# Optimization experiments

Measured on AMD Instinct MI355X. Metric: run time of the kernel, lower is better.

The kernel has to match this reference:

```python
import jax, jax.numpy as jnp
import numpy as np

N, M, C = 32768, 8192, 128
K = 3            # number of interpolation neighbors (PointNet++/RepSurf FP)
EPS_BN = 1e-5    # torch BatchNorm1d default eps
EPS_D = 1e-8     # RepSurf dist_recip eps


def setup_inputs() -> dict:
    key = jax.random.key(0)
    ks = jax.random.split(key, 16)
    s = 0.05
    inp = {
        "pos1": jax.random.normal(ks[0], (N, 3), jnp.float32),
        "pos2": jax.random.normal(ks[1], (M, 3), jnp.float32),
        "feat2": jax.random.normal(ks[2], (M, C), jnp.float32),
    }
    # MLP stack [128,128,128]: Linear + BatchNorm1d (gamma/beta) per layer
    for i in range(3):
        inp[f"W{i}"] = jax.random.normal(ks[3 + i], (C, C), jnp.float32) * s
        inp[f"b{i}"] = jnp.zeros((C,), jnp.float32)
        inp[f"g{i}"] = jnp.ones((C,), jnp.float32)
        inp[f"be{i}"] = jnp.zeros((C,), jnp.float32)
    return inp


def _lin_bn_relu(x, W, b, g, be):
    # Linear -> BatchNorm1d (training-mode batch stats, biased var) -> ReLU
    y = x @ W.T + b
    m = y.mean(axis=0)
    v = y.var(axis=0)
    return jax.nn.relu((y - m) * jax.lax.rsqrt(v + EPS_BN) * g + be)


def reference(pos1, pos2, feat2, W0, b0, g0, be0, W1, b1, g1, be1, W2, b2, g2, be2):
    # squared pairwise distances [N, M] (memory-bound: 1 GB fp32)
    d = ((pos1 ** 2).sum(-1, keepdims=True)
         + (pos2 ** 2).sum(-1)[None, :]
         - 2.0 * (pos1 @ pos2.T))
    neg_d, idx = jax.lax.top_k(-d, K)          # 3 nearest neighbors
    dk = jnp.maximum(-neg_d, 0.0)              # [N, K] squared dists
    w = 1.0 / (dk + EPS_D)
    w = w / w.sum(-1, keepdims=True)           # inverse-distance weights
    # gather neighbor features and interpolate: [N, K, C] -> [N, C]
    interp = jnp.einsum('nkc,nk->nc', feat2[idx], w)
    x = _lin_bn_relu(interp, W0, b0, g0, be0)
    x = _lin_bn_relu(x, W1, b1, g1, be1)
    x = _lin_bn_relu(x, W2, b2, g2, be2)
    return x
```

## Files before the change

### kernel.cpp

```cpp
#include <hip/hip_runtime.h>
#include <math.h>

#define NQ 32768
#define MC 8192
#define CC 128
#define EPS_BN 1e-5f
#define EPS_D  1e-8

#define DBL_BIG 1e300
#define IDX_BIG 0x7fffffff

#define QB  64
#define TB  512
#define NW  8
#define CH  2048
#define HM  (MC / 2)
#define NCH (HM / CH)
#define SLC (CH / NW)
#define KMASK 0xFFFFE000u
#define IMASK 0x1FFFu
#define NSURV 64
#define KNN_B ((NQ / QB) * 2)
#define GEMM_B (NQ / 64)
#define NGRP 8

typedef __attribute__((ext_vector_type(8))) short bf16x8;
typedef __attribute__((ext_vector_type(4))) float floatx4;
typedef unsigned short ushort_t;

__device__ __forceinline__ unsigned umin_(unsigned a, unsigned b) { return a < b ? a : b; }
__device__ __forceinline__ unsigned umax_(unsigned a, unsigned b) { return a > b ? a : b; }
#define KSWAP(a, b) { unsigned t_ = umin_(a, b); b = umax_(a, b); a = t_; }

__device__ __forceinline__ unsigned bf16pair(float a, float b) {
    unsigned ua = __float_as_uint(a); ua = (ua + 0x7FFFu + ((ua >> 16) & 1u)) >> 16;
    unsigned ub = __float_as_uint(b); ub = (ub + 0x7FFFu + ((ub >> 16) & 1u)) >> 16;
    return ua | (ub << 16);
}
__device__ __forceinline__ ushort_t bf16one(float a) {
    unsigned ua = __float_as_uint(a);
    return (ushort_t)((ua + 0x7FFFu + ((ua >> 16) & 1u)) >> 16);
}
__device__ __forceinline__ float bflo(unsigned u) { return __uint_as_float(u << 16); }
__device__ __forceinline__ float bfhi(unsigned u) { return __uint_as_float(u & 0xFFFF0000u); }

__global__ __launch_bounds__(TB) void knn_kernel(const float* __restrict__ pos1,
                                                 const float* __restrict__ pos2,
                                                 unsigned* __restrict__ skeys,
                                                 const float* __restrict__ W0,
                                                 const float* __restrict__ W1,
                                                 const float* __restrict__ W2,
                                                 ushort_t* __restrict__ Wbf,
                                                 float* __restrict__ stats) {
    __shared__ __align__(16) float4 sp4[CH * 3 / 4];
    __shared__ unsigned skey[QB][NW * 4];

    if (blockIdx.x >= KNN_B) {
        const int pb = blockIdx.x - KNN_B;
        const int f = pb * TB + threadIdx.x;
        const float* Ws[3] = {W0, W1, W2};
#pragma unroll
        for (int l = 0; l < 3; ++l) {
            const float4 v = ((const float4*)Ws[l])[f];
            unsigned* dst = (unsigned*)(Wbf + (size_t)l * CC * CC);
            dst[f * 2 + 0] = bf16pair(v.x, v.y);
            dst[f * 2 + 1] = bf16pair(v.z, v.w);
        }
        if (pb == 0)
            for (int i = threadIdx.x; i < 3 * NGRP * 256; i += TB) stats[i] = 0.f;
        return;
    }

    const int half = blockIdx.x & 1;
    const int bq   = blockIdx.x >> 1;
    const int wv = threadIdx.x >> 6;
    const int ln = threadIdx.x & 63;
    const int q  = bq * QB + ln;

    const float px = pos1[q * 3 + 0];
    const float py = pos1[q * 3 + 1];
    const float pz = pos1[q * 3 + 2];

    unsigned k0 = 0xFFFFFFFFu, k1 = 0xFFFFFFFFu, k2 = 0xFFFFFFFFu, k3 = 0xFFFFFFFFu;

    for (int c0 = 0; c0 < NCH; ++c0) {
        const int cb = half * HM + c0 * CH;
        __syncthreads();
        {
            const float4* g4 = (const float4*)(pos2 + (size_t)cb * 3);
#pragma unroll
            for (int i = threadIdx.x; i < CH * 3 / 4; i += TB) sp4[i] = g4[i];
        }
        __syncthreads();
        const float4* b4 = sp4 + wv * (SLC * 3 / 4);
        const int jb = cb + wv * SLC;
#pragma unroll 4
        for (int gi = 0; gi < SLC / 4; ++gi) {
            const float4 A = b4[gi * 3 + 0];
            const float4 B = b4[gi * 3 + 1];
            const float4 Cv = b4[gi * 3 + 2];
            const int j = jb + gi * 4;
            const float cx[4] = {A.x, A.w, B.z, Cv.y};
            const float cy[4] = {A.y, B.x, B.w, Cv.z};
            const float cz[4] = {A.z, B.y, Cv.x, Cv.w};
            unsigned e0, e1, e2, e3;
            {
                float dx = px - cx[0], dy = py - cy[0], dz = pz - cz[0];
                e0 = (__float_as_uint(fmaf(dx, dx, fmaf(dy, dy, dz * dz))) & KMASK) | (unsigned)(j + 0);
                dx = px - cx[1]; dy = py - cy[1]; dz = pz - cz[1];
                e1 = (__float_as_uint(fmaf(dx, dx, fmaf(dy, dy, dz * dz))) & KMASK) | (unsigned)(j + 1);
                dx = px - cx[2]; dy = py - cy[2]; dz = pz - cz[2];
                e2 = (__float_as_uint(fmaf(dx, dx, fmaf(dy, dy, dz * dz))) & KMASK) | (unsigned)(j + 2);
                dx = px - cx[3]; dy = py - cy[3]; dz = pz - cz[3];
                e3 = (__float_as_uint(fmaf(dx, dx, fmaf(dy, dy, dz * dz))) & KMASK) | (unsigned)(j + 3);
            }
            KSWAP(e0, e1); KSWAP(e2, e3); KSWAP(e0, e2); KSWAP(e1, e3); KSWAP(e1, e2);
            unsigned m0 = umin_(k0, e3), m1 = umin_(k1, e2);
            unsigned m2 = umin_(k2, e1), m3 = umin_(k3, e0);
            KSWAP(m0, m2); KSWAP(m1, m3); KSWAP(m0, m1); KSWAP(m2, m3);
            k0 = m0; k1 = m1; k2 = m2; k3 = m3;
        }
    }
    skey[ln][wv * 4 + 0] = k0;
    skey[ln][wv * 4 + 1] = k1;
    skey[ln][wv * 4 + 2] = k2;
    skey[ln][wv * 4 + 3] = k3;
    __syncthreads();

#pragma unroll
    for (int t = threadIdx.x * 4; t < threadIdx.x * 4 + 4; ++t) {
        const int ql = t >> 5, slot = t & 31;
        skeys[(size_t)(bq * QB + ql) * NSURV + half * 32 + slot] = skey[ql][slot];
    }
}

template <int MODE>
__global__ __launch_bounds__(256) void gemm_mfma(const void* __restrict__ Xsrc_,
                                                 const unsigned* __restrict__ skeys,
                                                 const float* __restrict__ pos1,
                                                 const float* __restrict__ pos2,
                                                 const float* __restrict__ statsIn,
                                                 const float* __restrict__ gIn,
                                                 const float* __restrict__ beIn,
                                                 const ushort_t* __restrict__ Wb,
                                                 const float* __restrict__ bias,
                                                 ushort_t* __restrict__ Y,
                                                 float* __restrict__ statsOut) {
    __shared__ __align__(16) short xa[64][136];
    __shared__ __align__(16) short wb[128][136];
    __shared__ float blk_s[CC], blk_q[CC];
    __shared__ float sc_l[CC], sh_l[CC];

    const int row0 = blockIdx.x * 64;

    if constexpr (MODE == 0) {
        const float* feat2 = (const float*)Xsrc_;
        __shared__ int   lidx[QB][3];
        __shared__ float lw[QB][3];
        {
            double* rrd = (double*)&xa[0][0];
            int*    rri = (int*)&wb[0][0];
            const int ql = threadIdx.x >> 2;
            const int pp = threadIdx.x & 3;
            const int qg = row0 + ql;
            const double qx = (double)pos1[qg * 3 + 0];
            const double qy = (double)pos1[qg * 3 + 1];
            const double qz = (double)pos1[qg * 3 + 2];
            double b0 = DBL_BIG, b1 = DBL_BIG, b2 = DBL_BIG;
            int    j0 = IDX_BIG, j1 = IDX_BIG, j2 = IDX_BIG;
            const uint4* kp = (const uint4*)(skeys + (size_t)qg * NSURV + pp * 16);
#pragma unroll
            for (int gi = 0; gi < 4; ++gi) {
                const uint4 kk = kp[gi];
                const unsigned ks[4] = {kk.x, kk.y, kk.z, kk.w};
#pragma unroll
                for (int u = 0; u < 4; ++u) {
                    const int id = (int)(ks[u] & IMASK);
                    const double x = (double)pos2[id * 3 + 0];
                    const double y = (double)pos2[id * 3 + 1];
                    const double z = (double)pos2[id * 3 + 2];
                    const double ax = qx - x, ay = qy - y, az = qz - z;
                    const double d = ax * ax + ay * ay + az * az;
                    const bool l2 = (d < b2) || (d == b2 && id < j2);
                    if (l2) {
                        const bool l1 = (d < b1) || (d == b1 && id < j1);
                        const bool l0 = (d < b0) || (d == b0 && id < j0);
                        b2 = l1 ? b1 : d;              j2 = l1 ? j1 : id;
                        b1 = l1 ? (l0 ? b0 : d) : b1;  j1 = l1 ? (l0 ? j0 : id) : j1;
                        b0 = l0 ? d : b0;              j0 = l0 ? id : j0;
                    }
                }
            }
            const int base = (ql * 4 + pp) * 3;
            rrd[base + 0] = b0; rri[base + 0] = j0;
            rrd[base + 1] = b1; rri[base + 1] = j1;
            rrd[base + 2] = b2; rri[base + 2] = j2;
            __syncthreads();
            if (threadIdx.x < QB) {
                const int qq = threadIdx.x;
                double c0 = DBL_BIG, c1 = DBL_BIG, c2 = DBL_BIG;
                int    i0 = IDX_BIG, i1 = IDX_BIG, i2 = IDX_BIG;
#pragma unroll
                for (int s = 0; s < 12; ++s) {
                    const double d = rrd[qq * 12 + s];
                    const int   id = rri[qq * 12 + s];
                    const bool l2 = (d < c2) || (d == c2 && id < i2);
                    if (l2) {
                        const bool l1 = (d < c1) || (d == c1 && id < i1);
                        const bool l0 = (d < c0) || (d == c0 && id < i0);
                        c2 = l1 ? c1 : d;              i2 = l1 ? i1 : id;
                        c1 = l1 ? (l0 ? c0 : d) : c1;  i1 = l1 ? (l0 ? i0 : id) : i1;
                        c0 = l0 ? d : c0;              i0 = l0 ? id : i0;
                    }
                }
                const double r0 = 1.0 / (c0 + EPS_D);
                const double r1 = 1.0 / (c1 + EPS_D);
                const double r2 = 1.0 / (c2 + EPS_D);
                const double inv = 1.0 / (r0 + r1 + r2);
                lidx[qq][0] = i0; lidx[qq][1] = i1; lidx[qq][2] = i2;
                lw[qq][0] = (float)(r0 * inv);
                lw[qq][1] = (float)(r1 * inv);
                lw[qq][2] = (float)(r2 * inv);
            }
            __syncthreads();
        }
        if (threadIdx.x < CC) { blk_s[threadIdx.x] = 0.f; blk_q[threadIdx.x] = 0.f; }
#pragma unroll
        for (int e = threadIdx.x; e < 64 * 32; e += 256) {
            const int r = e >> 5, c4 = e & 31;
            const int i0 = lidx[r][0], i1 = lidx[r][1], i2 = lidx[r][2];
            const float w0 = lw[r][0], w1 = lw[r][1], w2 = lw[r][2];
            const float4 f0 = *(const float4*)&feat2[(size_t)i0 * CC + c4 * 4];
            const float4 f1 = *(const float4*)&feat2[(size_t)i1 * CC + c4 * 4];
            const float4 f2 = *(const float4*)&feat2[(size_t)i2 * CC + c4 * 4];
            float4 v;
            v.x = w0 * f0.x + w1 * f1.x + w2 * f2.x;
            v.y = w0 * f0.y + w1 * f1.y + w2 * f2.y;
            v.z = w0 * f0.z + w1 * f1.z + w2 * f2.z;
            v.w = w0 * f0.w + w1 * f1.w + w2 * f2.w;
            unsigned* dst = (unsigned*)&xa[r][0];
            dst[c4 * 2 + 0] = bf16pair(v.x, v.y);
            dst[c4 * 2 + 1] = bf16pair(v.z, v.w);
        }
    } else {
        const ushort_t* Xbf = (const ushort_t*)Xsrc_;
        if (threadIdx.x < CC) {
            const int c = threadIdx.x;
            float s = 0.f, q = 0.f;
#pragma unroll
            for (int gr = 0; gr < NGRP; ++gr) {
                s += statsIn[gr * 256 + c];
                q += statsIn[gr * 256 + CC + c];
            }
            const float m = s * (1.f / (float)NQ);
            const float v = fmaf(-m, m, q * (1.f / (float)NQ));
            const float rstd = rsqrtf(v + EPS_BN);
            const float scl = gIn[c] * rstd;
            sc_l[c] = scl;
            sh_l[c] = fmaf(-m, scl, beIn[c]);
            blk_s[c] = 0.f; blk_q[c] = 0.f;
        }
        __syncthreads();
#pragma unroll
        for (int e = threadIdx.x; e < 64 * 16; e += 256) {
            const int r = e >> 4, c8 = e & 15;
            const uint4 u = *(const uint4*)&Xbf[(size_t)(row0 + r) * CC + c8 * 8];
            const float4 s0 = *(const float4*)&sc_l[c8 * 8];
            const float4 s1 = *(const float4*)&sc_l[c8 * 8 + 4];
            const float4 h0 = *(const float4*)&sh_l[c8 * 8];
            const float4 h1 = *(const float4*)&sh_l[c8 * 8 + 4];
            const float v0 = fmaxf(fmaf(bflo(u.x), s0.x, h0.x), 0.f);
            const float v1 = fmaxf(fmaf(bfhi(u.x), s0.y, h0.y), 0.f);
            const float v2 = fmaxf(fmaf(bflo(u.y), s0.z, h0.z), 0.f);
            const float v3 = fmaxf(fmaf(bfhi(u.y), s0.w, h0.w), 0.f);
            const float v4 = fmaxf(fmaf(bflo(u.z), s1.x, h1.x), 0.f);
            const float v5 = fmaxf(fmaf(bfhi(u.z), s1.y, h1.y), 0.f);
            const float v6 = fmaxf(fmaf(bflo(u.w), s1.z, h1.z), 0.f);
            const float v7 = fmaxf(fmaf(bfhi(u.w), s1.w, h1.w), 0.f);
            uint4 o;
            o.x = bf16pair(v0, v1); o.y = bf16pair(v2, v3);
            o.z = bf16pair(v4, v5); o.w = bf16pair(v6, v7);
            *(uint4*)&xa[r][c8 * 8] = o;
        }
    }
#pragma unroll
    for (int e = threadIdx.x; e < 128 * 16; e += 256) {
        const int co = e >> 4, seg = e & 15;
        *(float4*)&wb[co][seg * 8] = *(const float4*)&Wb[(size_t)co * CC + seg * 8];
    }
    __syncthreads();

    const int lane = threadIdx.x & 63;
    const int wv = threadIdx.x >> 6;
    const int nn = lane & 15;
    const int quad = lane >> 4;

    floatx4 acc[8] = {};

    const short* arow = &xa[wv * 16 + nn][0];
#pragma unroll
    for (int ks = 0; ks < 4; ++ks) {
        const bf16x8 a = *(const bf16x8*)(arow + ks * 32 + quad * 8);
#pragma unroll
        for (int ct = 0; ct < 8; ++ct) {
            const bf16x8 b = *(const bf16x8*)(&wb[ct * 16 + nn][0] + ks * 32 + quad * 8);
            acc[ct] = __builtin_amdgcn_mfma_f32_16x16x32_bf16(a, b, acc[ct], 0, 0, 0);
        }
    }

#pragma unroll
    for (int ct = 0; ct < 8; ++ct) {
        const float bv = bias[ct * 16 + nn];
        float s = 0.f, qv = 0.f;
#pragma unroll
        for (int r = 0; r < 4; ++r) {
            acc[ct][r] += bv;
            s += acc[ct][r];
            qv = fmaf(acc[ct][r], acc[ct][r], qv);
        }
#pragma unroll
        for (int r = 0; r < 4; ++r)
            Y[(size_t)(row0 + wv * 16 + quad * 4 + r) * CC + ct * 16 + nn] = bf16one(acc[ct][r]);
        s += __shfl_xor(s, 16, 64); s += __shfl_xor(s, 32, 64);
        qv += __shfl_xor(qv, 16, 64); qv += __shfl_xor(qv, 32, 64);
        if (quad == 0) {
            atomicAdd(&blk_s[ct * 16 + nn], s);
            atomicAdd(&blk_q[ct * 16 + nn], qv);
        }
    }
    __syncthreads();
    {
        const int ch = threadIdx.x;
        const float v = (ch < CC) ? blk_s[ch] : blk_q[ch - CC];
        atomicAdd(&statsOut[(blockIdx.x & (NGRP - 1)) * 256 + ch], v);
    }
}

__global__ __launch_bounds__(256) void bn_final(const ushort_t* __restrict__ Y,
                                                const float* __restrict__ statsIn,
                                                const float* __restrict__ g,
                                                const float* __restrict__ be,
                                                float* __restrict__ out) {
    __shared__ float sc_l[CC], sh_l[CC];
    if (threadIdx.x < CC) {
        const int c = threadIdx.x;
        float s = 0.f, q = 0.f;
#pragma unroll
        for (int gr = 0; gr < NGRP; ++gr) {
            s += statsIn[gr * 256 + c];
            q += statsIn[gr * 256 + CC + c];
        }
        const float m = s * (1.f / (float)NQ);
        const float v = fmaf(-m, m, q * (1.f / (float)NQ));
        const float rstd = rsqrtf(v + EPS_BN);
        const float scl = g[c] * rstd;
        sc_l[c] = scl;
        sh_l[c] = fmaf(-m, scl, be[c]);
    }
    __syncthreads();
    const int base = blockIdx.x * 1024 + threadIdx.x;
#pragma unroll
    for (int it = 0; it < 4; ++it) {
        const int i8 = base + it * 256;
        const int c8 = (i8 & 15) * 8;
        const uint4 u = *(const uint4*)&Y[(size_t)i8 * 8];
        const float4 s0 = *(const float4*)&sc_l[c8];
        const float4 s1 = *(const float4*)&sc_l[c8 + 4];
        const float4 h0 = *(const float4*)&sh_l[c8];
        const float4 h1 = *(const float4*)&sh_l[c8 + 4];
        float4 o0, o1;
        o0.x = fmaxf(fmaf(bflo(u.x), s0.x, h0.x), 0.f);
        o0.y = fmaxf(fmaf(bfhi(u.x), s0.y, h0.y), 0.f);
        o0.z = fmaxf(fmaf(bflo(u.y), s0.z, h0.z), 0.f);
        o0.w = fmaxf(fmaf(bfhi(u.y), s0.w, h0.w), 0.f);
        o1.x = fmaxf(fmaf(bflo(u.z), s1.x, h1.x), 0.f);
        o1.y = fmaxf(fmaf(bfhi(u.z), s1.y, h1.y), 0.f);
        o1.z = fmaxf(fmaf(bflo(u.w), s1.z, h1.z), 0.f);
        o1.w = fmaxf(fmaf(bfhi(u.w), s1.w, h1.w), 0.f);
        ((float4*)out)[i8 * 2 + 0] = o0;
        ((float4*)out)[i8 * 2 + 1] = o1;
    }
}

extern "C" void kernel_launch(void* const* d_in, const int* in_sizes, int n_in,
                              void* d_out, int out_size, void* d_ws, size_t ws_size,
                              hipStream_t stream) {
    (void)in_sizes; (void)n_in; (void)out_size; (void)ws_size;

    const float* pos1  = (const float*)d_in[0];
    const float* pos2  = (const float*)d_in[1];
    const float* feat2 = (const float*)d_in[2];
    const float* Wl[3]  = {(const float*)d_in[3], (const float*)d_in[7],  (const float*)d_in[11]};
    const float* bl[3]  = {(const float*)d_in[4], (const float*)d_in[8],  (const float*)d_in[12]};
    const float* gl[3]  = {(const float*)d_in[5], (const float*)d_in[9],  (const float*)d_in[13]};
    const float* bel[3] = {(const float*)d_in[6], (const float*)d_in[10], (const float*)d_in[14]};

    float* ws = (float*)d_ws;
    ushort_t* B0 = (ushort_t*)ws;
    ushort_t* B1 = B0 + (size_t)NQ * CC;
    unsigned* skeys = (unsigned*)(B1 + (size_t)NQ * CC);
    float* stats = (float*)(skeys + (size_t)NQ * NSURV);
    ushort_t* Wbf = (ushort_t*)(stats + 3 * NGRP * 256);

    float* st0 = stats + 0 * NGRP * 256;
    float* st1 = stats + 1 * NGRP * 256;
    float* st2 = stats + 2 * NGRP * 256;

    knn_kernel<<<KNN_B + 8, TB, 0, stream>>>(pos1, pos2, skeys,
                                             Wl[0], Wl[1], Wl[2], Wbf, stats);
    gemm_mfma<0><<<GEMM_B, 256, 0, stream>>>(feat2, skeys, pos1, pos2,
                                             nullptr, nullptr, nullptr,
                                             Wbf + 0 * CC * CC, bl[0], B0, st0);
    gemm_mfma<1><<<GEMM_B, 256, 0, stream>>>(B0, nullptr, nullptr, nullptr,
                                             st0, gl[0], bel[0],
                                             Wbf + 1 * CC * CC, bl[1], B1, st1);
    gemm_mfma<1><<<GEMM_B, 256, 0, stream>>>(B1, nullptr, nullptr, nullptr,
                                             st1, gl[1], bel[1],
                                             Wbf + 2 * CC * CC, bl[2], B0, st2);
    bn_final<<<GEMM_B, 256, 0, stream>>>(B0, st2, gl[2], bel[2], (float*)d_out);
}
```

Before: 204.6 us.

## Fuse three MLP layers and final BN into one persistent kernel with grid barriers

Replaces the three gemm launches and the final BN kernel with a single persistent kernel of 512 blocks. Each block keeps its 64-row activation tile in registers and LDS across layers and uses a software grid barrier on atomic counters to wait for the global BatchNorm statistics. This removes the bf16 intermediate round trips through global memory and three kernel launches. It depends on all 512 blocks being co-resident (launch_bounds 256,2), and the spin barrier adds synchronisation latency; the barrier counter is zeroed each call by the first kernel.

```diff
diff --git a/kernel.cpp b/kernel.cpp
--- a/kernel.cpp
+++ b/kernel.cpp
@@ -41,8 +41,6 @@
     unsigned ua = __float_as_uint(a);
     return (ushort_t)((ua + 0x7FFFu + ((ua >> 16) & 1u)) >> 16);
 }
-__device__ __forceinline__ float bflo(unsigned u) { return __uint_as_float(u << 16); }
-__device__ __forceinline__ float bfhi(unsigned u) { return __uint_as_float(u & 0xFFFF0000u); }
 
 __global__ __launch_bounds__(TB) void knn_kernel(const float* __restrict__ pos1,
                                                  const float* __restrict__ pos2,
@@ -67,7 +65,7 @@
             dst[f * 2 + 1] = bf16pair(v.z, v.w);
         }
         if (pb == 0)
-            for (int i = threadIdx.x; i < 3 * NGRP * 256; i += TB) stats[i] = 0.f;
+            for (int i = threadIdx.x; i < 3 * NGRP * 256 + 8; i += TB) stats[i] = 0.f;
         return;
     }
 
@@ -134,251 +132,270 @@
     }
 }
 
-template <int MODE>
-__global__ __launch_bounds__(256) void gemm_mfma(const void* __restrict__ Xsrc_,
-                                                 const unsigned* __restrict__ skeys,
-                                                 const float* __restrict__ pos1,
-                                                 const float* __restrict__ pos2,
-                                                 const float* __restrict__ statsIn,
-                                                 const float* __restrict__ gIn,
-                                                 const float* __restrict__ beIn,
-                                                 const ushort_t* __restrict__ Wb,
-                                                 const float* __restrict__ bias,
-                                                 ushort_t* __restrict__ Y,
-                                                 float* __restrict__ statsOut) {
+struct MlpP {
+    const float* feat2;
+    const unsigned* skeys;
+    const float* pos1;
+    const float* pos2;
+    const ushort_t* Wbf;
+    const float* bias0; const float* bias1; const float* bias2;
+    const float* g0;    const float* g1;    const float* g2;
+    const float* be0;   const float* be1;   const float* be2;
+    float* stats;
+    unsigned* bar;
+    float* out;
+};
+
+__device__ __forceinline__ void gbar(unsigned* cnt, unsigned* gen) {
+    __syncthreads();
+    if (threadIdx.x == 0) {
+        const unsigned g = __hip_atomic_load(gen, __ATOMIC_RELAXED, __HIP_MEMORY_SCOPE_AGENT);
+        const unsigned old = __hip_atomic_fetch_add(cnt, 1u, __ATOMIC_ACQ_REL, __HIP_MEMORY_SCOPE_AGENT);
+        if (old == (unsigned)(GEMM_B - 1)) {
+            __hip_atomic_store(cnt, 0u, __ATOMIC_RELAXED, __HIP_MEMORY_SCOPE_AGENT);
+            __hip_atomic_store(gen, g + 1u, __ATOMIC_RELEASE, __HIP_MEMORY_SCOPE_AGENT);
+        } else {
+            while (__hip_atomic_load(gen, __ATOMIC_ACQUIRE, __HIP_MEMORY_SCOPE_AGENT) == g)
+                __builtin_amdgcn_s_sleep(8);
+        }
+    }
+    __syncthreads();
+}
+
+__global__ __launch_bounds__(256, 2) void mlp_persist(MlpP P) {
     __shared__ __align__(16) short xa[64][136];
     __shared__ __align__(16) short wb[128][136];
     __shared__ float blk_s[CC], blk_q[CC];
     __shared__ float sc_l[CC], sh_l[CC];
+    __shared__ int   lidx[QB][3];
+    __shared__ float lw[QB][3];
 
     const int row0 = blockIdx.x * 64;
-
-    if constexpr (MODE == 0) {
-        const float* feat2 = (const float*)Xsrc_;
-        __shared__ int   lidx[QB][3];
-        __shared__ float lw[QB][3];
-        {
-            double* rrd = (double*)&xa[0][0];
-            int*    rri = (int*)&wb[0][0];
-            const int ql = threadIdx.x >> 2;
-            const int pp = threadIdx.x & 3;
-            const int qg = row0 + ql;
-            const double qx = (double)pos1[qg * 3 + 0];
-            const double qy = (double)pos1[qg * 3 + 1];
-            const double qz = (double)pos1[qg * 3 + 2];
-            double b0 = DBL_BIG, b1 = DBL_BIG, b2 = DBL_BIG;
-            int    j0 = IDX_BIG, j1 = IDX_BIG, j2 = IDX_BIG;
-            const uint4* kp = (const uint4*)(skeys + (size_t)qg * NSURV + pp * 16);
-#pragma unroll
-            for (int gi = 0; gi < 4; ++gi) {
-                const uint4 kk = kp[gi];
-                const unsigned ks[4] = {kk.x, kk.y, kk.z, kk.w};
-#pragma unroll
-                for (int u = 0; u < 4; ++u) {
-                    const int id = (int)(ks[u] & IMASK);
-                    const double x = (double)pos2[id * 3 + 0];
-                    const double y = (double)pos2[id * 3 + 1];
-                    const double z = (double)pos2[id * 3 + 2];
-                    const double ax = qx - x, ay = qy - y, az = qz - z;
-                    const double d = ax * ax + ay * ay + az * az;
-                    const bool l2 = (d < b2) || (d == b2 && id < j2);
-                    if (l2) {
-                        const bool l1 = (d < b1) || (d == b1 && id < j1);
-                        const bool l0 = (d < b0) || (d == b0 && id < j0);
-                        b2 = l1 ? b1 : d;              j2 = l1 ? j1 : id;
-                        b1 = l1 ? (l0 ? b0 : d) : b1;  j1 = l1 ? (l0 ? j0 : id) : j1;
-                        b0 = l0 ? d : b0;              j0 = l0 ? id : j0;
-                    }
-                }
-            }
-            const int base = (ql * 4 + pp) * 3;
-            rrd[base + 0] = b0; rri[base + 0] = j0;
-            rrd[base + 1] = b1; rri[base + 1] = j1;
-            rrd[base + 2] = b2; rri[base + 2] = j2;
-            __syncthreads();
-            if (threadIdx.x < QB) {
-                const int qq = threadIdx.x;
-                double c0 = DBL_BIG, c1 = DBL_BIG, c2 = DBL_BIG;
-                int    i0 = IDX_BIG, i1 = IDX_BIG, i2 = IDX_BIG;
-#pragma unroll
-                for (int s = 0; s < 12; ++s) {
-                    const double d = rrd[qq * 12 + s];
-                    const int   id = rri[qq * 12 + s];
-                    const bool l2 = (d < c2) || (d == c2 && id < i2);
-                    if (l2) {
-                        const bool l1 = (d < c1) || (d == c1 && id < i1);
-                        const bool l0 = (d < c0) || (d == c0 && id < i0);
-                        c2 = l1 ? c1 : d;              i2 = l1 ? i1 : id;
-                        c1 = l1 ? (l0 ? c0 : d) : c1;  i1 = l1 ? (l0 ? i0 : id) : i1;
-                        c0 = l0 ? d : c0;              i0 = l0 ? id : i0;
-                    }
-                }
-                const double r0 = 1.0 / (c0 + EPS_D);
-                const double r1 = 1.0 / (c1 + EPS_D);
-                const double r2 = 1.0 / (c2 + EPS_D);
-                const double inv = 1.0 / (r0 + r1 + r2);
-                lidx[qq][0] = i0; lidx[qq][1] = i1; lidx[qq][2] = i2;
-                lw[qq][0] = (float)(r0 * inv);
-                lw[qq][1] = (float)(r1 * inv);
-                lw[qq][2] = (float)(r2 * inv);
-            }
-            __syncthreads();
-        }
-        if (threadIdx.x < CC) { blk_s[threadIdx.x] = 0.f; blk_q[threadIdx.x] = 0.f; }
-#pragma unroll
-        for (int e = threadIdx.x; e < 64 * 32; e += 256) {
-            const int r = e >> 5, c4 = e & 31;
-            const int i0 = lidx[r][0], i1 = lidx[r][1], i2 = lidx[r][2];
-            const float w0 = lw[r][0], w1 = lw[r][1], w2 = lw[r][2];
-            const float4 f0 = *(const float4*)&feat2[(size_t)i0 * CC + c4 * 4];
-            const float4 f1 = *(const float4*)&feat2[(size_t)i1 * CC + c4 * 4];
-            const float4 f2 = *(const float4*)&feat2[(size_t)i2 * CC + c4 * 4];
-            float4 v;
-            v.x = w0 * f0.x + w1 * f1.x + w2 * f2.x;
-            v.y = w0 * f0.y + w1 * f1.y + w2 * f2.y;
-            v.z = w0 * f0.z + w1 * f1.z + w2 * f2.z;
-            v.w = w0 * f0.w + w1 * f1.w + w2 * f2.w;
-            unsigned* dst = (unsigned*)&xa[r][0];
-            dst[c4 * 2 + 0] = bf16pair(v.x, v.y);
-            dst[c4 * 2 + 1] = bf16pair(v.z, v.w);
-        }
-    } else {
-        const ushort_t* Xbf = (const ushort_t*)Xsrc_;
-        if (threadIdx.x < CC) {
-            const int c = threadIdx.x;
-            float s = 0.f, q = 0.f;
-#pragma unroll
-            for (int gr = 0; gr < NGRP; ++gr) {
-                s += statsIn[gr * 256 + c];
-                q += statsIn[gr * 256 + CC + c];
-            }
-            const float m = s * (1.f / (float)NQ);
-            const float v = fmaf(-m, m, q * (1.f / (float)NQ));
-            const float rstd = rsqrtf(v + EPS_BN);
-            const float scl = gIn[c] * rstd;
-            sc_l[c] = scl;
-            sh_l[c] = fmaf(-m, scl, beIn[c]);
-            blk_s[c] = 0.f; blk_q[c] = 0.f;
-        }
-        __syncthreads();
-#pragma unroll
-        for (int e = threadIdx.x; e < 64 * 16; e += 256) {
-            const int r = e >> 4, c8 = e & 15;
-            const uint4 u = *(const uint4*)&Xbf[(size_t)(row0 + r) * CC + c8 * 8];
-            const float4 s0 = *(const float4*)&sc_l[c8 * 8];
-            const float4 s1 = *(const float4*)&sc_l[c8 * 8 + 4];
-            const float4 h0 = *(const float4*)&sh_l[c8 * 8];
-            const float4 h1 = *(const float4*)&sh_l[c8 * 8 + 4];
-            const float v0 = fmaxf(fmaf(bflo(u.x), s0.x, h0.x), 0.f);
-            const float v1 = fmaxf(fmaf(bfhi(u.x), s0.y, h0.y), 0.f);
-            const float v2 = fmaxf(fmaf(bflo(u.y), s0.z, h0.z), 0.f);
-            const float v3 = fmaxf(fmaf(bfhi(u.y), s0.w, h0.w), 0.f);
-            const float v4 = fmaxf(fmaf(bflo(u.z), s1.x, h1.x), 0.f);
-            const float v5 = fmaxf(fmaf(bfhi(u.z), s1.y, h1.y), 0.f);
-            const float v6 = fmaxf(fmaf(bflo(u.w), s1.z, h1.z), 0.f);
-            const float v7 = fmaxf(fmaf(bfhi(u.w), s1.w, h1.w), 0.f);
-            uint4 o;
-            o.x = bf16pair(v0, v1); o.y = bf16pair(v2, v3);
-            o.z = bf16pair(v4, v5); o.w = bf16pair(v6, v7);
-            *(uint4*)&xa[r][c8 * 8] = o;
-        }
-    }
-#pragma unroll
-    for (int e = threadIdx.x; e < 128 * 16; e += 256) {
-        const int co = e >> 4, seg = e & 15;
-        *(float4*)&wb[co][seg * 8] = *(const float4*)&Wb[(size_t)co * CC + seg * 8];
-    }
-    __syncthreads();
-
     const int lane = threadIdx.x & 63;
     const int wv = threadIdx.x >> 6;
     const int nn = lane & 15;
     const int quad = lane >> 4;
 
-    floatx4 acc[8] = {};
-
-    const short* arow = &xa[wv * 16 + nn][0];
-#pragma unroll
-    for (int ks = 0; ks < 4; ++ks) {
-        const bf16x8 a = *(const bf16x8*)(arow + ks * 32 + quad * 8);
+    {
+        double* rrd = (double*)&xa[0][0];
+        int*    rri = (int*)&wb[0][0];
+        const int ql = threadIdx.x >> 2;
+        const int pp = threadIdx.x & 3;
+        const int qg = row0 + ql;
+        const double qx = (double)P.pos1[qg * 3 + 0];
+        const double qy = (double)P.pos1[qg * 3 + 1];
+        const double qz = (double)P.pos1[qg * 3 + 2];
+        double b0 = DBL_BIG, b1 = DBL_BIG, b2 = DBL_BIG;
+        int    j0 = IDX_BIG, j1 = IDX_BIG, j2 = IDX_BIG;
+        const uint4* kp = (const uint4*)(P.skeys + (size_t)qg * NSURV + pp * 16);
+#pragma unroll
+        for (int gi = 0; gi < 4; ++gi) {
+            const uint4 kk = kp[gi];
+            const unsigned ks[4] = {kk.x, kk.y, kk.z, kk.w};
+#pragma unroll
+            for (int u = 0; u < 4; ++u) {
+                const int id = (int)(ks[u] & IMASK);
+                const double x = (double)P.pos2[id * 3 + 0];
+                const double y = (double)P.pos2[id * 3 + 1];
+                const double z = (double)P.pos2[id * 3 + 2];
+                const double ax = qx - x, ay = qy - y, az = qz - z;
+                const double d = ax * ax + ay * ay + az * az;
+                const bool l2 = (d < b2) || (d == b2 && id < j2);
+                if (l2) {
+                    const bool l1 = (d < b1) || (d == b1 && id < j1);
+                    const bool l0 = (d < b0) || (d == b0 && id < j0);
+                    b2 = l1 ? b1 : d;              j2 = l1 ? j1 : id;
+                    b1 = l1 ? (l0 ? b0 : d) : b1;  j1 = l1 ? (l0 ? j0 : id) : j1;
+                    b0 = l0 ? d : b0;              j0 = l0 ? id : j0;
+                }
+            }
+        }
+        const int base = (ql * 4 + pp) * 3;
+        rrd[base + 0] = b0; rri[base + 0] = j0;
+        rrd[base + 1] = b1; rri[base + 1] = j1;
+        rrd[base + 2] = b2; rri[base + 2] = j2;
+        __syncthreads();
+        if (threadIdx.x < QB) {
+            const int qq = threadIdx.x;
+            double c0 = DBL_BIG, c1 = DBL_BIG, c2 = DBL_BIG;
+            int    i0 = IDX_BIG, i1 = IDX_BIG, i2 = IDX_BIG;
+#pragma unroll
+            for (int s = 0; s < 12; ++s) {
+                const double d = rrd[qq * 12 + s];
+                const int   id = rri[qq * 12 + s];
+                const bool l2 = (d < c2) || (d == c2 && id < i2);
+                if (l2) {
+                    const bool l1 = (d < c1) || (d == c1 && id < i1);
+                    const bool l0 = (d < c0) || (d == c0 && id < i0);
+                    c2 = l1 ? c1 : d;              i2 = l1 ? i1 : id;
+                    c1 = l1 ? (l0 ? c0 : d) : c1;  i1 = l1 ? (l0 ? i0 : id) : i1;
+                    c0 = l0 ? d : c0;              i0 = l0 ? id : i0;
+                }
+            }
+            const double r0 = 1.0 / (c0 + EPS_D);
+            const double r1 = 1.0 / (c1 + EPS_D);
+            const double r2 = 1.0 / (c2 + EPS_D);
+            const double inv = 1.0 / (r0 + r1 + r2);
+            lidx[qq][0] = i0; lidx[qq][1] = i1; lidx[qq][2] = i2;
+            lw[qq][0] = (float)(r0 * inv);
+            lw[qq][1] = (float)(r1 * inv);
+            lw[qq][2] = (float)(r2 * inv);
+        }
+        __syncthreads();
+    }
+
+#pragma unroll
+    for (int e = threadIdx.x; e < 64 * 32; e += 256) {
+        const int r = e >> 5, c4 = e & 31;
+        const int i0 = lidx[r][0], i1 = lidx[r][1], i2 = lidx[r][2];
+        const float w0 = lw[r][0], w1 = lw[r][1], w2 = lw[r][2];
+        const float4 f0 = *(const float4*)&P.feat2[(size_t)i0 * CC + c4 * 4];
+        const float4 f1 = *(const float4*)&P.feat2[(size_t)i1 * CC + c4 * 4];
+        const float4 f2 = *(const float4*)&P.feat2[(size_t)i2 * CC + c4 * 4];
+        float4 v;
+        v.x = w0 * f0.x + w1 * f1.x + w2 * f2.x;
+        v.y = w0 * f0.y + w1 * f1.y + w2 * f2.y;
+        v.z = w0 * f0.z + w1 * f1.z + w2 * f2.z;
+        v.w = w0 * f0.w + w1 * f1.w + w2 * f2.w;
+        unsigned* dst = (unsigned*)&xa[r][0];
+        dst[c4 * 2 + 0] = bf16pair(v.x, v.y);
+        dst[c4 * 2 + 1] = bf16pair(v.z, v.w);
+    }
+#pragma unroll
+    for (int e = threadIdx.x; e < 128 * 16; e += 256) {
+        const int co = e >> 4, seg = e & 15;
+        *(float4*)&wb[co][seg * 8] = *(const float4*)&P.Wbf[(size_t)co * CC + seg * 8];
+    }
+    __syncthreads();
+
+    const float* biasL[3] = {P.bias0, P.bias1, P.bias2};
+    const float* gL[3]    = {P.g0, P.g1, P.g2};
+    const float* beL[3]   = {P.be0, P.be1, P.be2};
+
+    floatx4 acc[8];
+#pragma unroll
+    for (int ct = 0; ct < 8; ++ct) acc[ct] = (floatx4){0.f, 0.f, 0.f, 0.f};
+    {
+        const short* arow = &xa[wv * 16 + nn][0];
+#pragma unroll
+        for (int ks = 0; ks < 4; ++ks) {
+            const bf16x8 a = *(const bf16x8*)(arow + ks * 32 + quad * 8);
+#pragma unroll
+            for (int ct = 0; ct < 8; ++ct) {
+                const bf16x8 b = *(const bf16x8*)(&wb[ct * 16 + nn][0] + ks * 32 + quad * 8);
+                acc[ct] = __builtin_amdgcn_mfma_f32_16x16x32_bf16(a, b, acc[ct], 0, 0, 0);
+            }
+        }
 #pragma unroll
         for (int ct = 0; ct < 8; ++ct) {
-            const bf16x8 b = *(const bf16x8*)(&wb[ct * 16 + nn][0] + ks * 32 + quad * 8);
-            acc[ct] = __builtin_amdgcn_mfma_f32_16x16x32_bf16(a, b, acc[ct], 0, 0, 0);
-        }
-    }
-
-#pragma unroll
-    for (int ct = 0; ct < 8; ++ct) {
-        const float bv = bias[ct * 16 + nn];
-        float s = 0.f, qv = 0.f;
-#pragma unroll
-        for (int r = 0; r < 4; ++r) {
-            acc[ct][r] += bv;
-            s += acc[ct][r];
-            qv = fmaf(acc[ct][r], acc[ct][r], qv);
-        }
-#pragma unroll
-        for (int r = 0; r < 4; ++r)
-            Y[(size_t)(row0 + wv * 16 + quad * 4 + r) * CC + ct * 16 + nn] = bf16one(acc[ct][r]);
-        s += __shfl_xor(s, 16, 64); s += __shfl_xor(s, 32, 64);
-        qv += __shfl_xor(qv, 16, 64); qv += __shfl_xor(qv, 32, 64);
-        if (quad == 0) {
-            atomicAdd(&blk_s[ct * 16 + nn], s);
-            atomicAdd(&blk_q[ct * 16 + nn], qv);
-        }
-    }
-    __syncthreads();
-    {
-        const int ch = threadIdx.x;
-        const float v = (ch < CC) ? blk_s[ch] : blk_q[ch - CC];
-        atomicAdd(&statsOut[(blockIdx.x & (NGRP - 1)) * 256 + ch], v);
-    }
-}
-
-__global__ __launch_bounds__(256) void bn_final(const ushort_t* __restrict__ Y,
-                                                const float* __restrict__ statsIn,
-                                                const float* __restrict__ g,
-                                                const float* __restrict__ be,
-                                                float* __restrict__ out) {
-    __shared__ float sc_l[CC], sh_l[CC];
-    if (threadIdx.x < CC) {
-        const int c = threadIdx.x;
-        float s = 0.f, q = 0.f;
-#pragma unroll
-        for (int gr = 0; gr < NGRP; ++gr) {
-            s += statsIn[gr * 256 + c];
-            q += statsIn[gr * 256 + CC + c];
-        }
-        const float m = s * (1.f / (float)NQ);
-        const float v = fmaf(-m, m, q * (1.f / (float)NQ));
-        const float rstd = rsqrtf(v + EPS_BN);
-        const float scl = g[c] * rstd;
-        sc_l[c] = scl;
-        sh_l[c] = fmaf(-m, scl, be[c]);
-    }
-    __syncthreads();
-    const int base = blockIdx.x * 1024 + threadIdx.x;
-#pragma unroll
-    for (int it = 0; it < 4; ++it) {
-        const int i8 = base + it * 256;
-        const int c8 = (i8 & 15) * 8;
-        const uint4 u = *(const uint4*)&Y[(size_t)i8 * 8];
-        const float4 s0 = *(const float4*)&sc_l[c8];
-        const float4 s1 = *(const float4*)&sc_l[c8 + 4];
-        const float4 h0 = *(const float4*)&sh_l[c8];
-        const float4 h1 = *(const float4*)&sh_l[c8 + 4];
-        float4 o0, o1;
-        o0.x = fmaxf(fmaf(bflo(u.x), s0.x, h0.x), 0.f);
-        o0.y = fmaxf(fmaf(bfhi(u.x), s0.y, h0.y), 0.f);
-        o0.z = fmaxf(fmaf(bflo(u.y), s0.z, h0.z), 0.f);
-        o0.w = fmaxf(fmaf(bfhi(u.y), s0.w, h0.w), 0.f);
-        o1.x = fmaxf(fmaf(bflo(u.z), s1.x, h1.x), 0.f);
-        o1.y = fmaxf(fmaf(bfhi(u.z), s1.y, h1.y), 0.f);
-        o1.z = fmaxf(fmaf(bflo(u.w), s1.z, h1.z), 0.f);
-        o1.w = fmaxf(fmaf(bfhi(u.w), s1.w, h1.w), 0.f);
-        ((float4*)out)[i8 * 2 + 0] = o0;
-        ((float4*)out)[i8 * 2 + 1] = o1;
+            const float bv = biasL[0][ct * 16 + nn];
+#pragma unroll
+            for (int r = 0; r < 4; ++r) acc[ct][r] += bv;
+        }
+    }
+
+    for (int l = 0; l < 3; ++l) {
+        float* stL = P.stats + l * NGRP * 256;
+        __syncthreads();
+        if (threadIdx.x < CC) { blk_s[threadIdx.x] = 0.f; blk_q[threadIdx.x] = 0.f; }
+        __syncthreads();
+#pragma unroll
+        for (int ct = 0; ct < 8; ++ct) {
+            float s = 0.f, qv = 0.f;
+#pragma unroll
+            for (int r = 0; r < 4; ++r) {
+                s += acc[ct][r];
+                qv = fmaf(acc[ct][r], acc[ct][r], qv);
+            }
+            s += __shfl_xor(s, 16, 64); s += __shfl_xor(s, 32, 64);
+            qv += __shfl_xor(qv, 16, 64); qv += __shfl_xor(qv, 32, 64);
+            if (quad == 0) {
+                atomicAdd(&blk_s[ct * 16 + nn], s);
+                atomicAdd(&blk_q[ct * 16 + nn], qv);
+            }
+        }
+        __syncthreads();
+        {
+            const int ch = threadIdx.x;
+            const float v = (ch < CC) ? blk_s[ch] : blk_q[ch - CC];
+            atomicAdd(&stL[(blockIdx.x & (NGRP - 1)) * 256 + ch], v);
+        }
+        gbar(P.bar, P.bar + 1);
+        if (threadIdx.x < CC) {
+            const int c = threadIdx.x;
+            float s = 0.f, q = 0.f;
+#pragma unroll
+            for (int gr = 0; gr < NGRP; ++gr) {
+                s += stL[gr * 256 + c];
+                q += stL[gr * 256 + CC + c];
+            }
+            const float m = s * (1.f / (float)NQ);
+            const float v = fmaf(-m, m, q * (1.f / (float)NQ));
+            const float rstd = rsqrtf(v + EPS_BN);
+            const float scl = gL[l][c] * rstd;
+            sc_l[c] = scl;
+            sh_l[c] = fmaf(-m, scl, beL[l][c]);
+        }
+        __syncthreads();
+
+        if (l < 2) {
+#pragma unroll
+            for (int ct = 0; ct < 8; ++ct) {
+                const int col = ct * 16 + nn;
+                const float scl = sc_l[col], shf = sh_l[col];
+#pragma unroll
+                for (int r = 0; r < 4; ++r) {
+                    const int row = wv * 16 + quad * 4 + r;
+                    const float v = fmaxf(fmaf(acc[ct][r], scl, shf), 0.f);
+                    ((ushort_t*)&xa[row][0])[col] = bf16one(v);
+                }
+            }
+            const ushort_t* Wp = P.Wbf + (size_t)(l + 1) * CC * CC;
+#pragma unroll
+            for (int e = threadIdx.x; e < 128 * 16; e += 256) {
+                const int co = e >> 4, seg = e & 15;
+                *(float4*)&wb[co][seg * 8] = *(const float4*)&Wp[(size_t)co * CC + seg * 8];
+            }
+            __syncthreads();
+#pragma unroll
+            for (int ct = 0; ct < 8; ++ct) acc[ct] = (floatx4){0.f, 0.f, 0.f, 0.f};
+            const short* arow = &xa[wv * 16 + nn][0];
+#pragma unroll
+            for (int ks = 0; ks < 4; ++ks) {
+                const bf16x8 a = *(const bf16x8*)(arow + ks * 32 + quad * 8);
+#pragma unroll
+                for (int ct = 0; ct < 8; ++ct) {
+                    const bf16x8 b = *(const bf16x8*)(&wb[ct * 16 + nn][0] + ks * 32 + quad * 8);
+                    acc[ct] = __builtin_amdgcn_mfma_f32_16x16x32_bf16(a, b, acc[ct], 0, 0, 0);
+                }
+            }
+#pragma unroll
+            for (int ct = 0; ct < 8; ++ct) {
+                const float bv = biasL[l + 1][ct * 16 + nn];
+#pragma unroll
+                for (int r = 0; r < 4; ++r) acc[ct][r] += bv;
+            }
+        } else {
+            float* wf = (float*)&wb[0][0];
+#pragma unroll
+            for (int ct = 0; ct < 8; ++ct) {
+                const int col = ct * 16 + nn;
+                const float scl = sc_l[col], shf = sh_l[col];
+#pragma unroll
+                for (int r = 0; r < 4; ++r) {
+                    const int row = wv * 16 + quad * 4 + r;
+                    wf[row * 132 + col] = fmaxf(fmaf(acc[ct][r], scl, shf), 0.f);
+                }
+            }
+            __syncthreads();
+#pragma unroll
+            for (int it = 0; it < 8; ++it) {
+                const int idx = it * 256 + threadIdx.x;
+                const int row = idx >> 5, c4 = idx & 31;
+                const float4 v = *(const float4*)&wf[row * 132 + c4 * 4];
+                *(float4*)&P.out[(size_t)(row0 + row) * CC + c4 * 4] = v;
+            }
+        }
     }
 }
 
@@ -396,26 +413,19 @@
     const float* bel[3] = {(const float*)d_in[6], (const float*)d_in[10], (const float*)d_in[14]};
 
     float* ws = (float*)d_ws;
-    ushort_t* B0 = (ushort_t*)ws;
-    ushort_t* B1 = B0 + (size_t)NQ * CC;
-    unsigned* skeys = (unsigned*)(B1 + (size_t)NQ * CC);
+    unsigned* skeys = (unsigned*)ws;
     float* stats = (float*)(skeys + (size_t)NQ * NSURV);
-    ushort_t* Wbf = (ushort_t*)(stats + 3 * NGRP * 256);
-
-    float* st0 = stats + 0 * NGRP * 256;
-    float* st1 = stats + 1 * NGRP * 256;
-    float* st2 = stats + 2 * NGRP * 256;
+    unsigned* bar = (unsigned*)(stats + 3 * NGRP * 256);
+    ushort_t* Wbf = (ushort_t*)(stats + 3 * NGRP * 256 + 8);
 
     knn_kernel<<<KNN_B + 8, TB, 0, stream>>>(pos1, pos2, skeys,
                                              Wl[0], Wl[1], Wl[2], Wbf, stats);
-    gemm_mfma<0><<<GEMM_B, 256, 0, stream>>>(feat2, skeys, pos1, pos2,
-                                             nullptr, nullptr, nullptr,
-                                             Wbf + 0 * CC * CC, bl[0], B0, st0);
-    gemm_mfma<1><<<GEMM_B, 256, 0, stream>>>(B0, nullptr, nullptr, nullptr,
-                                             st0, gl[0], bel[0],
-                                             Wbf + 1 * CC * CC, bl[1], B1, st1);
-    gemm_mfma<1><<<GEMM_B, 256, 0, stream>>>(B1, nullptr, nullptr, nullptr,
-                                             st1, gl[1], bel[1],
-                                             Wbf + 2 * CC * CC, bl[2], B0, st2);
-    bn_final<<<GEMM_B, 256, 0, stream>>>(B0, st2, gl[2], bel[2], (float*)d_out);
-}
+    MlpP P;
+    P.feat2 = feat2; P.skeys = skeys; P.pos1 = pos1; P.pos2 = pos2;
+    P.Wbf = Wbf;
+    P.bias0 = bl[0]; P.bias1 = bl[1]; P.bias2 = bl[2];
+    P.g0 = gl[0]; P.g1 = gl[1]; P.g2 = gl[2];
+    P.be0 = bel[0]; P.be1 = bel[1]; P.be2 = bel[2];
+    P.stats = stats; P.bar = bar; P.out = (float*)d_out;
+    mlp_persist<<<GEMM_B, 256, 0, stream>>>(P);
+}
```

Measured after the change: 310.2 us. 51.6% more time.
